# Optimization experiments

Measured on AMD Instinct MI355X. Metric: run time of the kernel, lower is better.

Reference implementation:

```python
import jax, jax.numpy as jnp
import numpy as np

N, D, H = 4096, 1024, 16
GAMMA = 1.0


def setup_inputs() -> dict:
    key = jax.random.key(0)
    ks = jax.random.split(key, 10)
    s = 1.0 / np.sqrt(D)
    return {
        "x": jax.random.normal(ks[0], (N, D), jnp.float32),
        "h": jax.random.normal(ks[1], (N,), jnp.float32),
        "Wq": jax.random.normal(ks[2], (D, D), jnp.float32) * s,
        "bq": jax.random.normal(ks[3], (D,), jnp.float32) * s,
        "Wk": jax.random.normal(ks[4], (D, D), jnp.float32) * s,
        "bk": jax.random.normal(ks[5], (D,), jnp.float32) * s,
        "Wv": jax.random.normal(ks[6], (D, D), jnp.float32) * s,
        "bv": jax.random.normal(ks[7], (D,), jnp.float32) * s,
        "Wo": jax.random.normal(ks[8], (D, D), jnp.float32) * s,
        "bo": jax.random.normal(ks[9], (D,), jnp.float32) * s,
    }


def reference(x, h, Wq, bq, Wk, bk, Wv, bv, Wo, bo):
    n, d = x.shape
    d_head = d // H
    # torch Linear: y = x @ W.T + b
    q = (x @ Wq.T + bq).reshape(n, H, d_head)
    k = (x @ Wk.T + bk).reshape(n, H, d_head)
    v = (x @ Wv.T + bv).reshape(n, H, d_head)
    scale = 1.0 / np.sqrt(d_head).astype(np.float32)
    logits = jnp.einsum('nhd,mhd->hnm', q, k) * scale  # (H, n, n)
    logits = logits - (GAMMA * h)[None, None, :]       # per-key additive bias
    attn = jax.nn.softmax(logits, axis=-1)
    out = jnp.einsum('hnm,mhd->nhd', attn, v).reshape(n, d)
    return out @ Wo.T + bo + x
```

## Files before the change

kernel.cpp:

```cpp
#include <hip/hip_runtime.h>
#include <hip/hip_bf16.h>
#include <stdint.h>

#define NTOK 4096
#define DM   1024
#define NH   16
#define DH   64
#define SCL  0.1803368801111129f
#define LOG2E 1.4426950408889634f

typedef __attribute__((ext_vector_type(8)))  short bf16x8;
typedef __attribute__((ext_vector_type(4)))  float f32x4;
typedef __attribute__((ext_vector_type(16))) float f32x16;
typedef __attribute__((ext_vector_type(4)))  unsigned short us4;

__device__ inline unsigned short f2bf(float f) {
  union { float f; unsigned int u; } a;
  a.f = f;
  unsigned int u = a.u;
  u += 0x7fffu + ((u >> 16) & 1u);
  return (unsigned short)(u >> 16);
}

__device__ inline unsigned int cvtpk_bf16(float lo, float hi) {
  unsigned int r;
  asm("v_cvt_pk_bf16_f32 %0, %1, %2" : "=v"(r) : "v"(lo), "v"(hi));
  return r;
}

__device__ inline void gload_lds16(const void* gsrc, void* ldst) {
  __builtin_amdgcn_global_load_lds(
      (const __attribute__((address_space(1))) void*)(uintptr_t)gsrc,
      (__attribute__((address_space(3))) void*)(unsigned int)(uintptr_t)ldst,
      16, 0, 0);
}

__global__ void cvt_fused(const float* __restrict__ x,
                          const float* __restrict__ Wq,
                          const float* __restrict__ Wk,
                          const float* __restrict__ Wv,
                          const float* __restrict__ Wo,
                          const float* __restrict__ h,
                          unsigned short* __restrict__ xb,
                          unsigned short* __restrict__ wqkvb,
                          unsigned short* __restrict__ wob,
                          float* __restrict__ hperm) {
  const int b = blockIdx.x;
  if (b >= 8192) {
    int i = (b - 8192) * 256 + threadIdx.x;
    int r  = i & 15;
    int hh = (i >> 4) & 1;
    int t  = i >> 5;
    int key = t * 32 + (r & 3) + 8 * (r >> 2) + 4 * hh;
    hperm[i] = -LOG2E * h[key];
    return;
  }
  int i = b * 256 + threadIdx.x;
  const float* src; unsigned short* dst; int off;
  if (i < 1048576)      { src = x;  dst = xb;                 off = i; }
  else if (i < 1310720) { src = Wq; dst = wqkvb;              off = i - 1048576; }
  else if (i < 1572864) { src = Wk; dst = wqkvb + DM * DM;    off = i - 1310720; }
  else if (i < 1835008) { src = Wv; dst = wqkvb + 2 * DM * DM; off = i - 1572864; }
  else                  { src = Wo; dst = wob;                off = i - 1835008; }
  float4 v = ((const float4*)src)[off];
  us4 o;
  o[0] = f2bf(v.x); o[1] = f2bf(v.y); o[2] = f2bf(v.z); o[3] = f2bf(v.w);
  ((us4*)dst)[off] = o;
}

__global__ __launch_bounds__(256)
void gemm_qkv(const unsigned short* __restrict__ A,
              const unsigned short* __restrict__ B,
              const float* __restrict__ bq, const float* __restrict__ bk,
              const float* __restrict__ bv,
              unsigned short* __restrict__ Qb, unsigned short* __restrict__ Kb,
              unsigned short* __restrict__ Vt)
{
  const int bid = blockIdx.x;
  const int wg  = (bid & 7) * 96 + (bid >> 3);
  const int bn  = (wg % 24) * 128;
  const int bm  = (wg / 24) * 128;
  const int tid  = threadIdx.x;
  const int wid  = tid >> 6;
  const int lane = tid & 63;
  const int wr = wid >> 1;
  const int wc = wid & 1;

  __shared__ __align__(16) unsigned short As[2][128 * 32];
  __shared__ __align__(16) unsigned short Bs[2][128 * 32];

  f32x4 acc[4][4];
#pragma unroll
  for (int i = 0; i < 4; i++)
#pragma unroll
    for (int j = 0; j < 4; j++) acc[i][j] = f32x4{0.f, 0.f, 0.f, 0.f};

  const int fr = lane & 15;
  const int fk = (lane >> 4) * 8;
  const int srow = lane >> 2;
  const int scol = (lane & 3) * 8;

  for (int k0 = 0; k0 < DM; k0 += 64) {
#pragma unroll
    for (int half = 0; half < 2; ++half) {
#pragma unroll
      for (int c = 0; c < 2; ++c) {
        const int chunk = wid * 2 + c;
        gload_lds16(A + (size_t)(bm + chunk * 16 + srow) * DM + k0 + half * 32 + scol,
                    &As[half][chunk * 512]);
        gload_lds16(B + (size_t)(bn + chunk * 16 + srow) * DM + k0 + half * 32 + scol,
                    &Bs[half][chunk * 512]);
      }
    }
    __syncthreads();
#pragma unroll
    for (int half = 0; half < 2; ++half) {
      bf16x8 af[4], bfr[4];
#pragma unroll
      for (int i = 0; i < 4; i++)
        af[i] = *(const bf16x8*)&As[half][(wr * 64 + i * 16 + fr) * 32 + fk];
#pragma unroll
      for (int j = 0; j < 4; j++)
        bfr[j] = *(const bf16x8*)&Bs[half][(wc * 64 + j * 16 + fr) * 32 + fk];
#pragma unroll
      for (int i = 0; i < 4; i++)
#pragma unroll
        for (int j = 0; j < 4; j++)
          acc[i][j] = __builtin_amdgcn_mfma_f32_16x16x32_bf16(af[i], bfr[j],
                                                              acc[i][j], 0, 0, 0);
    }
    __syncthreads();
  }

  const int fq = lane >> 4;
  const int region = bn >> 10;
  const float* bias = (region == 0) ? bq : (region == 1) ? bk : bv;
  const float qscale = (region == 0) ? SCL : 1.0f;
  unsigned short* outp = (region == 0) ? Qb : Kb;
#pragma unroll
  for (int j = 0; j < 4; j++) {
    const int col = bn + wc * 64 + j * 16 + fr;
    const int cl  = col & 1023;
    const float bvx = bias[cl];
#pragma unroll
    for (int i = 0; i < 4; i++) {
      const int row0 = bm + wr * 64 + i * 16 + fq * 4;
      if (region < 2) {
#pragma unroll
        for (int r = 0; r < 4; r++)
          outp[(size_t)(row0 + r) * DM + cl] = f2bf((acc[i][j][r] + bvx) * qscale);
      } else {
        us4 pk;
#pragma unroll
        for (int r = 0; r < 4; r++) pk[r] = f2bf(acc[i][j][r] + bvx);
        *(us4*)&Vt[(size_t)cl * NTOK + row0] = pk;
      }
    }
  }
}

__global__ __launch_bounds__(256)
void gemm_out(const unsigned short* __restrict__ A,
              const unsigned short* __restrict__ B,
              const float* __restrict__ bias,
              const float* __restrict__ resid,
              float* __restrict__ Cf)
{
  const int bid = blockIdx.x;
  const int wg  = (bid & 7) * 64 + (bid >> 3);
  const int bn  = (wg % 16) * 64;
  const int bm  = (wg / 16) * 128;
  const int tid  = threadIdx.x;
  const int wid  = tid >> 6;
  const int lane = tid & 63;

  __shared__ __align__(16) unsigned short As[128 * 32];
  __shared__ __align__(16) unsigned short Bs[64 * 32];

  f32x4 acc[2][4];
#pragma unroll
  for (int i = 0; i < 2; i++)
#pragma unroll
    for (int j = 0; j < 4; j++) acc[i][j] = f32x4{0.f, 0.f, 0.f, 0.f};

  const int fr = lane & 15;
  const int fk = (lane >> 4) * 8;
  const int srow = lane >> 2;
  const int scol = (lane & 3) * 8;

  for (int k0 = 0; k0 < DM; k0 += 32) {
#pragma unroll
    for (int c = 0; c < 3; ++c) {
      const int chunk = wid * 3 + c;
      if (chunk < 8) {
        gload_lds16(A + (size_t)(bm + chunk * 16 + srow) * DM + k0 + scol,
                    &As[chunk * 512]);
      } else {
        gload_lds16(B + (size_t)(bn + (chunk - 8) * 16 + srow) * DM + k0 + scol,
                    &Bs[(chunk - 8) * 512]);
      }
    }
    __syncthreads();
    bf16x8 af[2], bfr[4];
#pragma unroll
    for (int i = 0; i < 2; i++)
      af[i] = *(const bf16x8*)&As[(wid * 32 + i * 16 + fr) * 32 + fk];
#pragma unroll
    for (int j = 0; j < 4; j++)
      bfr[j] = *(const bf16x8*)&Bs[(j * 16 + fr) * 32 + fk];
#pragma unroll
    for (int i = 0; i < 2; i++)
#pragma unroll
      for (int j = 0; j < 4; j++)
        acc[i][j] = __builtin_amdgcn_mfma_f32_16x16x32_bf16(af[i], bfr[j],
                                                            acc[i][j], 0, 0, 0);
    __syncthreads();
  }

  const int fq = lane >> 4;
#pragma unroll
  for (int j = 0; j < 4; j++) {
    const int col = bn + j * 16 + fr;
    const float bvx = bias[col];
#pragma unroll
    for (int i = 0; i < 2; i++) {
      const int row0 = bm + wid * 32 + i * 16 + fq * 4;
#pragma unroll
      for (int r = 0; r < 4; r++) {
        const size_t idx = (size_t)(row0 + r) * DM + col;
        Cf[idx] = acc[i][j][r] + bvx + resid[idx];
      }
    }
  }
}

#define MFMA32(a, b, c) __builtin_amdgcn_mfma_f32_32x32x16_bf16(a, b, c, 0, 0, 0)

__global__ __launch_bounds__(512)
void attn_kernel(const unsigned short* __restrict__ Q,
                 const unsigned short* __restrict__ K,
                 const unsigned short* __restrict__ Vt,
                 const float* __restrict__ hperm,
                 unsigned short* __restrict__ O)
{
  const int wgid = (blockIdx.x & 7) * 64 + (blockIdx.x >> 3);
  const int head = wgid >> 5;
  const int qblk = wgid & 31;
  const int tid  = threadIdx.x;
  const int wid  = tid >> 6;
  const int grp  = wid >> 2;
  const int w4   = wid & 3;
  const int lane = tid & 63;
  const int c31  = lane & 31;
  const int hi   = lane >> 5;
  const int qwb  = qblk * 128 + w4 * 32;
  const int k0g  = grp * 2048;

  __shared__ __align__(16) char lds_raw[32768];
  char* kbase = lds_raw + grp * 16384;
  char* vbase = kbase + 8192;

  const int srow = w4 * 4 + (lane >> 4);
  const int ssl  = lane & 15;
  const int sq   = ssl ^ srow;
  const int kkey = srow + 16 * (sq >> 3);
  const unsigned short* kg =
      K + (size_t)(k0g + kkey) * DM + head * DH + (sq & 7) * 8;
  const int vd = (sq >> 2) * 16 + srow;
  const unsigned short* vg =
      Vt + (size_t)(head * DH + vd) * NTOK + k0g + (sq & 3) * 8;

  const int fr15 = c31 & 15;
  const int fkh  = c31 >> 4;
  int koffB[4], voffB[2][2];
#pragma unroll
  for (int f = 0; f < 4; f++)
    koffB[f] = fr15 * 256 + (((fkh * 8 + f * 2 + hi) ^ fr15) << 4);
#pragma unroll
  for (int db = 0; db < 2; db++)
#pragma unroll
    for (int ko = 0; ko < 2; ko++)
      voffB[db][ko] =
          fr15 * 256 + ((((db * 2 + fkh) * 4 + ko * 2 + hi) ^ fr15) << 4);

  const unsigned short* qp = Q + (size_t)(qwb + c31) * DM + head * DH + hi * 8;
  const bf16x8 qf0 = *(const bf16x8*)(qp);
  const bf16x8 qf1 = *(const bf16x8*)(qp + 16);
  const bf16x8 qf2 = *(const bf16x8*)(qp + 32);
  const bf16x8 qf3 = *(const bf16x8*)(qp + 48);

  f32x16 o0, o1;
#pragma unroll
  for (int i = 0; i < 16; i++) { o0[i] = 0.f; o1[i] = 0.f; }
  float l = 0.f;

  gload_lds16(kg, kbase + w4 * 1024);
  gload_lds16(vg, vbase + w4 * 1024);
  __syncthreads();

  int cur = 0;
  const int NT = 2048 / 32;
  for (int t = 0; t < NT; ++t) {
    if (t + 1 < NT) {
      gload_lds16(kg + (size_t)(t + 1) * 32 * DM,
                  kbase + (cur ^ 1) * 4096 + w4 * 1024);
      gload_lds16(vg + (t + 1) * 32,
                  vbase + (cur ^ 1) * 4096 + w4 * 1024);
    }

    const float* hp = hperm + k0g + t * 32 + hi * 16;
    const float4 b0 = *(const float4*)(hp + 0);
    const float4 b1 = *(const float4*)(hp + 4);
    const float4 b2 = *(const float4*)(hp + 8);
    const float4 b3 = *(const float4*)(hp + 12);

    const char* Kb = kbase + cur * 4096;
    const char* Vb = vbase + cur * 4096;
    const bf16x8 kf0 = *(const bf16x8*)(Kb + koffB[0]);
    const bf16x8 kf1 = *(const bf16x8*)(Kb + koffB[1]);
    const bf16x8 kf2 = *(const bf16x8*)(Kb + koffB[2]);
    const bf16x8 kf3 = *(const bf16x8*)(Kb + koffB[3]);

    f32x16 s;
    s[0]  = b0.x; s[1]  = b0.y; s[2]  = b0.z; s[3]  = b0.w;
    s[4]  = b1.x; s[5]  = b1.y; s[6]  = b1.z; s[7]  = b1.w;
    s[8]  = b2.x; s[9]  = b2.y; s[10] = b2.z; s[11] = b2.w;
    s[12] = b3.x; s[13] = b3.y; s[14] = b3.z; s[15] = b3.w;

    s = MFMA32(kf0, qf0, s);
    s = MFMA32(kf1, qf1, s);
    s = MFMA32(kf2, qf2, s);
    s = MFMA32(kf3, qf3, s);

    const bf16x8 v00 = *(const bf16x8*)(Vb + voffB[0][0]);
    const bf16x8 v01 = *(const bf16x8*)(Vb + voffB[0][1]);
    const bf16x8 v10 = *(const bf16x8*)(Vb + voffB[1][0]);
    const bf16x8 v11 = *(const bf16x8*)(Vb + voffB[1][1]);

    float ps[16];
#pragma unroll
    for (int r = 0; r < 16; r++) ps[r] = __builtin_amdgcn_exp2f(s[r]);
    l += (((ps[0] + ps[1]) + (ps[2] + ps[3])) +
          ((ps[4] + ps[5]) + (ps[6] + ps[7]))) +
         (((ps[8] + ps[9]) + (ps[10] + ps[11])) +
          ((ps[12] + ps[13]) + (ps[14] + ps[15])));

    unsigned int X1 = cvtpk_bf16(ps[0],  ps[1]);
    unsigned int X2 = cvtpk_bf16(ps[2],  ps[3]);
    unsigned int Y1 = cvtpk_bf16(ps[4],  ps[5]);
    unsigned int Y2 = cvtpk_bf16(ps[6],  ps[7]);
    asm("v_permlane32_swap_b32 %0, %1" : "+v"(X1), "+v"(Y1));
    asm("v_permlane32_swap_b32 %0, %1" : "+v"(X2), "+v"(Y2));
    unsigned int X3 = cvtpk_bf16(ps[8],  ps[9]);
    unsigned int X4 = cvtpk_bf16(ps[10], ps[11]);
    unsigned int Y3 = cvtpk_bf16(ps[12], ps[13]);
    unsigned int Y4 = cvtpk_bf16(ps[14], ps[15]);
    asm("v_permlane32_swap_b32 %0, %1" : "+v"(X3), "+v"(Y3));
    asm("v_permlane32_swap_b32 %0, %1" : "+v"(X4), "+v"(Y4));

    union { unsigned int u[4]; bf16x8 v; } P0, P1;
    P0.u[0] = X1; P0.u[1] = X2; P0.u[2] = Y1; P0.u[3] = Y2;
    P1.u[0] = X3; P1.u[1] = X4; P1.u[2] = Y3; P1.u[3] = Y4;

    o0 = MFMA32(v00, P0.v, o0);
    o0 = MFMA32(v01, P1.v, o0);
    o1 = MFMA32(v10, P0.v, o1);
    o1 = MFMA32(v11, P1.v, o1);

    __syncthreads();
    cur ^= 1;
  }

  l += __shfl_xor(l, 32, 64);

  float* mo = (float*)lds_raw;
  float* mL = (float*)(lds_raw + 17408);
  float* row = &mo[(w4 * 64 + lane) * 17];
#pragma unroll
  for (int half = 0; half < 2; half++) {
    __syncthreads();
    if (grp == 1) {
      const f32x16& hA = half ? o1 : o0;
#pragma unroll
      for (int i = 0; i < 16; i++) row[i] = hA[i];
      if (half == 0 && hi == 0) mL[w4 * 32 + c31] = l;
    }
    __syncthreads();
    if (grp == 0) {
      f32x16& hA = half ? o1 : o0;
#pragma unroll
      for (int i = 0; i < 16; i++) hA[i] += row[i];
      if (half == 0) l += mL[w4 * 32 + c31];
    }
  }

  if (grp == 0) {
    const float inv = 1.0f / l;
    unsigned short* ob = O + (size_t)(qwb + c31) * DM + head * DH;
#pragma unroll
    for (int g = 0; g < 4; g++) {
      us4 pk;
      pk[0] = f2bf(o0[4 * g + 0] * inv); pk[1] = f2bf(o0[4 * g + 1] * inv);
      pk[2] = f2bf(o0[4 * g + 2] * inv); pk[3] = f2bf(o0[4 * g + 3] * inv);
      *(us4*)(ob + 8 * g + 4 * hi) = pk;
      pk[0] = f2bf(o1[4 * g + 0] * inv); pk[1] = f2bf(o1[4 * g + 1] * inv);
      pk[2] = f2bf(o1[4 * g + 2] * inv); pk[3] = f2bf(o1[4 * g + 3] * inv);
      *(us4*)(ob + 32 + 8 * g + 4 * hi) = pk;
    }
  }
}

extern "C" void kernel_launch(void* const* d_in, const int* in_sizes, int n_in,
                              void* d_out, int out_size, void* d_ws, size_t ws_size,
                              hipStream_t stream) {
  const float* x  = (const float*)d_in[0];
  const float* h  = (const float*)d_in[1];
  const float* Wq = (const float*)d_in[2];
  const float* bq = (const float*)d_in[3];
  const float* Wk = (const float*)d_in[4];
  const float* bk = (const float*)d_in[5];
  const float* Wv = (const float*)d_in[6];
  const float* bv = (const float*)d_in[7];
  const float* Wo = (const float*)d_in[8];
  const float* bo = (const float*)d_in[9];
  float* out = (float*)d_out;

  char* ws = (char*)d_ws;
  const size_t MB = 1 << 20;
  unsigned short* xb    = (unsigned short*)(ws + 0 * MB);
  unsigned short* wqkvb = (unsigned short*)(ws + 8 * MB);
  unsigned short* wob   = (unsigned short*)(ws + 14 * MB);
  unsigned short* Qb    = (unsigned short*)(ws + 16 * MB);
  unsigned short* Kb    = (unsigned short*)(ws + 24 * MB);
  unsigned short* Vtb   = (unsigned short*)(ws + 32 * MB);
  unsigned short* AOb   = (unsigned short*)(ws + 40 * MB);
  float*          hperm = (float*)(ws + 48 * MB);

  cvt_fused<<<8208, 256, 0, stream>>>(x, Wq, Wk, Wv, Wo, h,
                                      xb, wqkvb, wob, hperm);

  gemm_qkv<<<768, 256, 0, stream>>>(xb, wqkvb, bq, bk, bv, Qb, Kb, Vtb);

  attn_kernel<<<dim3(512), 512, 0, stream>>>(Qb, Kb, Vtb, hperm, AOb);

  gemm_out<<<512, 256, 0, stream>>>(AOb, wob, bo, x, out);
}
```

Before: 167.2 us.

## Double K-tile depth in attention and out-proj GEMM, read bf16 residual

The attention loop now stages 64 keys per iteration (two 32-key passes) and the output GEMM loads 64 K-elements per barrier. This halves the number of __syncthreads and global-load rounds per block. The residual add in the output projection reads the bf16 copy of x instead of fp32 to cut memory traffic. In exchange, LDS usage doubles, which can lower occupancy, and the residual loses precision.

```diff
diff --git a/kernel.cpp b/kernel.cpp
--- a/kernel.cpp
+++ b/kernel.cpp
@@ -20,6 +20,12 @@
   unsigned int u = a.u;
   u += 0x7fffu + ((u >> 16) & 1u);
   return (unsigned short)(u >> 16);
+}
+
+__device__ inline float bf2f(unsigned short v) {
+  union { unsigned int u; float f; } a;
+  a.u = ((unsigned int)v) << 16;
+  return a.f;
 }
 
 __device__ inline unsigned int cvtpk_bf16(float lo, float hi) {
@@ -163,7 +169,7 @@
 void gemm_out(const unsigned short* __restrict__ A,
               const unsigned short* __restrict__ B,
               const float* __restrict__ bias,
-              const float* __restrict__ resid,
+              const unsigned short* __restrict__ residb,
               float* __restrict__ Cf)
 {
   const int bid = blockIdx.x;
@@ -174,8 +180,8 @@
   const int wid  = tid >> 6;
   const int lane = tid & 63;
 
-  __shared__ __align__(16) unsigned short As[128 * 32];
-  __shared__ __align__(16) unsigned short Bs[64 * 32];
+  __shared__ __align__(16) unsigned short As[2][128 * 32];
+  __shared__ __align__(16) unsigned short Bs[2][64 * 32];
 
   f32x4 acc[2][4];
 #pragma unroll
@@ -188,32 +194,38 @@
   const int srow = lane >> 2;
   const int scol = (lane & 3) * 8;
 
-  for (int k0 = 0; k0 < DM; k0 += 32) {
-#pragma unroll
-    for (int c = 0; c < 3; ++c) {
-      const int chunk = wid * 3 + c;
-      if (chunk < 8) {
-        gload_lds16(A + (size_t)(bm + chunk * 16 + srow) * DM + k0 + scol,
-                    &As[chunk * 512]);
-      } else {
-        gload_lds16(B + (size_t)(bn + (chunk - 8) * 16 + srow) * DM + k0 + scol,
-                    &Bs[(chunk - 8) * 512]);
+  for (int k0 = 0; k0 < DM; k0 += 64) {
+#pragma unroll
+    for (int half = 0; half < 2; ++half) {
+#pragma unroll
+      for (int c = 0; c < 3; ++c) {
+        const int chunk = wid * 3 + c;
+        if (chunk < 8) {
+          gload_lds16(A + (size_t)(bm + chunk * 16 + srow) * DM + k0 + half * 32 + scol,
+                      &As[half][chunk * 512]);
+        } else {
+          gload_lds16(B + (size_t)(bn + (chunk - 8) * 16 + srow) * DM + k0 + half * 32 + scol,
+                      &Bs[half][(chunk - 8) * 512]);
+        }
       }
     }
     __syncthreads();
-    bf16x8 af[2], bfr[4];
-#pragma unroll
-    for (int i = 0; i < 2; i++)
-      af[i] = *(const bf16x8*)&As[(wid * 32 + i * 16 + fr) * 32 + fk];
-#pragma unroll
-    for (int j = 0; j < 4; j++)
-      bfr[j] = *(const bf16x8*)&Bs[(j * 16 + fr) * 32 + fk];
-#pragma unroll
-    for (int i = 0; i < 2; i++)
+#pragma unroll
+    for (int half = 0; half < 2; ++half) {
+      bf16x8 af[2], bfr[4];
+#pragma unroll
+      for (int i = 0; i < 2; i++)
+        af[i] = *(const bf16x8*)&As[half][(wid * 32 + i * 16 + fr) * 32 + fk];
 #pragma unroll
       for (int j = 0; j < 4; j++)
-        acc[i][j] = __builtin_amdgcn_mfma_f32_16x16x32_bf16(af[i], bfr[j],
-                                                            acc[i][j], 0, 0, 0);
+        bfr[j] = *(const bf16x8*)&Bs[half][(j * 16 + fr) * 32 + fk];
+#pragma unroll
+      for (int i = 0; i < 2; i++)
+#pragma unroll
+        for (int j = 0; j < 4; j++)
+          acc[i][j] = __builtin_amdgcn_mfma_f32_16x16x32_bf16(af[i], bfr[j],
+                                                              acc[i][j], 0, 0, 0);
+    }
     __syncthreads();
   }
 
@@ -228,7 +240,7 @@
 #pragma unroll
       for (int r = 0; r < 4; r++) {
         const size_t idx = (size_t)(row0 + r) * DM + col;
-        Cf[idx] = acc[i][j][r] + bvx + resid[idx];
+        Cf[idx] = acc[i][j][r] + bvx + bf2f(residb[idx]);
       }
     }
   }
@@ -256,9 +268,9 @@
   const int qwb  = qblk * 128 + w4 * 32;
   const int k0g  = grp * 2048;
 
-  __shared__ __align__(16) char lds_raw[32768];
-  char* kbase = lds_raw + grp * 16384;
-  char* vbase = kbase + 8192;
+  __shared__ __align__(16) char lds_raw[65536];
+  char* kbase = lds_raw + grp * 32768;
+  char* vbase = kbase + 16384;
 
   const int srow = w4 * 4 + (lane >> 4);
   const int ssl  = lane & 15;
@@ -294,78 +306,85 @@
   for (int i = 0; i < 16; i++) { o0[i] = 0.f; o1[i] = 0.f; }
   float l = 0.f;
 
-  gload_lds16(kg, kbase + w4 * 1024);
-  gload_lds16(vg, vbase + w4 * 1024);
+  gload_lds16(kg,                      kbase + w4 * 1024);
+  gload_lds16(kg + (size_t)32 * DM,    kbase + 4096 + w4 * 1024);
+  gload_lds16(vg,                      vbase + w4 * 1024);
+  gload_lds16(vg + 32,                 vbase + 4096 + w4 * 1024);
   __syncthreads();
 
   int cur = 0;
-  const int NT = 2048 / 32;
+  const int NT = 2048 / 64;
   for (int t = 0; t < NT; ++t) {
     if (t + 1 < NT) {
-      gload_lds16(kg + (size_t)(t + 1) * 32 * DM,
-                  kbase + (cur ^ 1) * 4096 + w4 * 1024);
-      gload_lds16(vg + (t + 1) * 32,
-                  vbase + (cur ^ 1) * 4096 + w4 * 1024);
-    }
-
-    const float* hp = hperm + k0g + t * 32 + hi * 16;
-    const float4 b0 = *(const float4*)(hp + 0);
-    const float4 b1 = *(const float4*)(hp + 4);
-    const float4 b2 = *(const float4*)(hp + 8);
-    const float4 b3 = *(const float4*)(hp + 12);
-
-    const char* Kb = kbase + cur * 4096;
-    const char* Vb = vbase + cur * 4096;
-    const bf16x8 kf0 = *(const bf16x8*)(Kb + koffB[0]);
-    const bf16x8 kf1 = *(const bf16x8*)(Kb + koffB[1]);
-    const bf16x8 kf2 = *(const bf16x8*)(Kb + koffB[2]);
-    const bf16x8 kf3 = *(const bf16x8*)(Kb + koffB[3]);
-
-    f32x16 s;
-    s[0]  = b0.x; s[1]  = b0.y; s[2]  = b0.z; s[3]  = b0.w;
-    s[4]  = b1.x; s[5]  = b1.y; s[6]  = b1.z; s[7]  = b1.w;
-    s[8]  = b2.x; s[9]  = b2.y; s[10] = b2.z; s[11] = b2.w;
-    s[12] = b3.x; s[13] = b3.y; s[14] = b3.z; s[15] = b3.w;
-
-    s = MFMA32(kf0, qf0, s);
-    s = MFMA32(kf1, qf1, s);
-    s = MFMA32(kf2, qf2, s);
-    s = MFMA32(kf3, qf3, s);
-
-    const bf16x8 v00 = *(const bf16x8*)(Vb + voffB[0][0]);
-    const bf16x8 v01 = *(const bf16x8*)(Vb + voffB[0][1]);
-    const bf16x8 v10 = *(const bf16x8*)(Vb + voffB[1][0]);
-    const bf16x8 v11 = *(const bf16x8*)(Vb + voffB[1][1]);
-
-    float ps[16];
-#pragma unroll
-    for (int r = 0; r < 16; r++) ps[r] = __builtin_amdgcn_exp2f(s[r]);
-    l += (((ps[0] + ps[1]) + (ps[2] + ps[3])) +
-          ((ps[4] + ps[5]) + (ps[6] + ps[7]))) +
-         (((ps[8] + ps[9]) + (ps[10] + ps[11])) +
-          ((ps[12] + ps[13]) + (ps[14] + ps[15])));
-
-    unsigned int X1 = cvtpk_bf16(ps[0],  ps[1]);
-    unsigned int X2 = cvtpk_bf16(ps[2],  ps[3]);
-    unsigned int Y1 = cvtpk_bf16(ps[4],  ps[5]);
-    unsigned int Y2 = cvtpk_bf16(ps[6],  ps[7]);
-    asm("v_permlane32_swap_b32 %0, %1" : "+v"(X1), "+v"(Y1));
-    asm("v_permlane32_swap_b32 %0, %1" : "+v"(X2), "+v"(Y2));
-    unsigned int X3 = cvtpk_bf16(ps[8],  ps[9]);
-    unsigned int X4 = cvtpk_bf16(ps[10], ps[11]);
-    unsigned int Y3 = cvtpk_bf16(ps[12], ps[13]);
-    unsigned int Y4 = cvtpk_bf16(ps[14], ps[15]);
-    asm("v_permlane32_swap_b32 %0, %1" : "+v"(X3), "+v"(Y3));
-    asm("v_permlane32_swap_b32 %0, %1" : "+v"(X4), "+v"(Y4));
-
-    union { unsigned int u[4]; bf16x8 v; } P0, P1;
-    P0.u[0] = X1; P0.u[1] = X2; P0.u[2] = Y1; P0.u[3] = Y2;
-    P1.u[0] = X3; P1.u[1] = X4; P1.u[2] = Y3; P1.u[3] = Y4;
-
-    o0 = MFMA32(v00, P0.v, o0);
-    o0 = MFMA32(v01, P1.v, o0);
-    o1 = MFMA32(v10, P0.v, o1);
-    o1 = MFMA32(v11, P1.v, o1);
+      const unsigned short* kn = kg + (size_t)(t + 1) * 64 * DM;
+      const unsigned short* vn = vg + (t + 1) * 64;
+      gload_lds16(kn,                   kbase + (cur ^ 1) * 8192 + w4 * 1024);
+      gload_lds16(kn + (size_t)32 * DM, kbase + (cur ^ 1) * 8192 + 4096 + w4 * 1024);
+      gload_lds16(vn,                   vbase + (cur ^ 1) * 8192 + w4 * 1024);
+      gload_lds16(vn + 32,              vbase + (cur ^ 1) * 8192 + 4096 + w4 * 1024);
+    }
+
+#pragma unroll
+    for (int pass = 0; pass < 2; ++pass) {
+      const float* hp = hperm + k0g + t * 64 + pass * 32 + hi * 16;
+      const float4 b0 = *(const float4*)(hp + 0);
+      const float4 b1 = *(const float4*)(hp + 4);
+      const float4 b2 = *(const float4*)(hp + 8);
+      const float4 b3 = *(const float4*)(hp + 12);
+
+      const char* Kb = kbase + cur * 8192 + pass * 4096;
+      const char* Vb = vbase + cur * 8192 + pass * 4096;
+      const bf16x8 kf0 = *(const bf16x8*)(Kb + koffB[0]);
+      const bf16x8 kf1 = *(const bf16x8*)(Kb + koffB[1]);
+      const bf16x8 kf2 = *(const bf16x8*)(Kb + koffB[2]);
+      const bf16x8 kf3 = *(const bf16x8*)(Kb + koffB[3]);
+
+      f32x16 s;
+      s[0]  = b0.x; s[1]  = b0.y; s[2]  = b0.z; s[3]  = b0.w;
+      s[4]  = b1.x; s[5]  = b1.y; s[6]  = b1.z; s[7]  = b1.w;
+      s[8]  = b2.x; s[9]  = b2.y; s[10] = b2.z; s[11] = b2.w;
+      s[12] = b3.x; s[13] = b3.y; s[14] = b3.z; s[15] = b3.w;
+
+      s = MFMA32(kf0, qf0, s);
+      s = MFMA32(kf1, qf1, s);
+      s = MFMA32(kf2, qf2, s);
+      s = MFMA32(kf3, qf3, s);
+
+      const bf16x8 v00 = *(const bf16x8*)(Vb + voffB[0][0]);
+      const bf16x8 v01 = *(const bf16x8*)(Vb + voffB[0][1]);
+      const bf16x8 v10 = *(const bf16x8*)(Vb + voffB[1][0]);
+      const bf16x8 v11 = *(const bf16x8*)(Vb + voffB[1][1]);
+
+      float ps[16];
+#pragma unroll
+      for (int r = 0; r < 16; r++) ps[r] = __builtin_amdgcn_exp2f(s[r]);
+      l += (((ps[0] + ps[1]) + (ps[2] + ps[3])) +
+            ((ps[4] + ps[5]) + (ps[6] + ps[7]))) +
+           (((ps[8] + ps[9]) + (ps[10] + ps[11])) +
+            ((ps[12] + ps[13]) + (ps[14] + ps[15])));
+
+      unsigned int X1 = cvtpk_bf16(ps[0],  ps[1]);
+      unsigned int X2 = cvtpk_bf16(ps[2],  ps[3]);
+      unsigned int Y1 = cvtpk_bf16(ps[4],  ps[5]);
+      unsigned int Y2 = cvtpk_bf16(ps[6],  ps[7]);
+      asm("v_permlane32_swap_b32 %0, %1" : "+v"(X1), "+v"(Y1));
+      asm("v_permlane32_swap_b32 %0, %1" : "+v"(X2), "+v"(Y2));
+      unsigned int X3 = cvtpk_bf16(ps[8],  ps[9]);
+      unsigned int X4 = cvtpk_bf16(ps[10], ps[11]);
+      unsigned int Y3 = cvtpk_bf16(ps[12], ps[13]);
+      unsigned int Y4 = cvtpk_bf16(ps[14], ps[15]);
+      asm("v_permlane32_swap_b32 %0, %1" : "+v"(X3), "+v"(Y3));
+      asm("v_permlane32_swap_b32 %0, %1" : "+v"(X4), "+v"(Y4));
+
+      union { unsigned int u[4]; bf16x8 v; } P0, P1;
+      P0.u[0] = X1; P0.u[1] = X2; P0.u[2] = Y1; P0.u[3] = Y2;
+      P1.u[0] = X3; P1.u[1] = X4; P1.u[2] = Y3; P1.u[3] = Y4;
+
+      o0 = MFMA32(v00, P0.v, o0);
+      o0 = MFMA32(v01, P1.v, o0);
+      o1 = MFMA32(v10, P0.v, o1);
+      o1 = MFMA32(v11, P1.v, o1);
+    }
 
     __syncthreads();
     cur ^= 1;
@@ -443,5 +462,5 @@
 
   attn_kernel<<<dim3(512), 512, 0, stream>>>(Qb, Kb, Vtb, hperm, AOb);
 
-  gemm_out<<<512, 256, 0, stream>>>(AOb, wob, bo, x, out);
-}
+  gemm_out<<<512, 256, 0, stream>>>(AOb, wob, bo, xb, out);
+}
```

Result: no change. 166.1 us (-0.7%).
